# Optimization experiments

Measured on AMD Instinct MI355X. Metric: run time of the kernel, lower is better.

The kernel has to match this reference:

```python
import jax, jax.numpy as jnp
import numpy as np

B, S, D, H = 2, 2048, 2048, 16
HD = D // H
QMAX = 127.0  # 8-bit activation quant


def ste_round(x):
    # forward: round; backward: identity
    return x + jax.lax.stop_gradient(jnp.round(x) - x)


def bitlinear(x, w):
    """BitNet b1.58 linear: per-tensor ternary weights + per-token int8 activations.

    x: [..., in], w: [out, in] -> [..., out]
    """
    w_scale = jnp.maximum(jnp.mean(jnp.abs(w)), 1e-6)
    w_q = jnp.clip(ste_round(w / w_scale), -1.0, 1.0)          # ternary {-1,0,1}
    a_max = jnp.clip(jnp.max(jnp.abs(x), axis=-1, keepdims=True), 1e-8, None)
    x_q = jnp.clip(ste_round(x * (QMAX / a_max)), -QMAX, QMAX)  # int8 range
    y = jnp.einsum('bsi,oi->bso', x_q, w_q)
    return y * (w_scale * a_max / QMAX)


def setup_inputs() -> dict:
    key = jax.random.key(0)
    ks = jax.random.split(key, 5)
    std = 1.0 / np.sqrt(D)  # muP-style init from BitLinear
    return {
        'x': jax.random.normal(ks[0], (B, S, D), dtype=jnp.float32),
        'wq': jax.random.normal(ks[1], (D, D), dtype=jnp.float32) * std,
        'wk': jax.random.normal(ks[2], (D, D), dtype=jnp.float32) * std,
        'wv': jax.random.normal(ks[3], (D, D), dtype=jnp.float32) * std,
        'wo': jax.random.normal(ks[4], (D, D), dtype=jnp.float32) * std,
    }


def reference(x, wq, wk, wv, wo):
    q = bitlinear(x, wq).reshape(B, S, H, HD)
    k = bitlinear(x, wk).reshape(B, S, H, HD)
    v = bitlinear(x, wv).reshape(B, S, H, HD)
    scores = jnp.einsum('bqhd,bkhd->bhqk', q, k) / np.sqrt(HD)
    # causal mask
    causal = jnp.tril(jnp.ones((S, S), dtype=bool))
    scores = jnp.where(causal[None, None], scores, jnp.finfo(scores.dtype).min)
    attn = jax.nn.softmax(scores, axis=-1)
    ctx = jnp.einsum('bhqk,bkhd->bqhd', attn, v).reshape(B, S, D)
    return bitlinear(ctx, wo)
```

## Files before the change

kernel.cpp:

```cpp
#include <hip/hip_runtime.h>
#include <hip/hip_bf16.h>
#include <cstdint>
#include <cstddef>


#define BB 2
#define SS 2048
#define DD 2048
#define HH 16
#define HDD 128
#define MM (BB*SS)

typedef __attribute__((ext_vector_type(8))) short bf16x8;
typedef __attribute__((ext_vector_type(4))) float f32x4;
typedef __attribute__((ext_vector_type(16))) float f32x16;
typedef __attribute__((ext_vector_type(4))) int   i32x4;
typedef unsigned short u16;
typedef unsigned int   u32;
typedef unsigned char  u8;
typedef signed char    s8;

#define MFMA(a,b,c)   __builtin_amdgcn_mfma_f32_16x16x32_bf16(a,b,c,0,0,0)
#define MFMA32(a,b,c) __builtin_amdgcn_mfma_f32_32x32x16_bf16(a,b,c,0,0,0)
#define MFMAI8(a,b,c) __builtin_amdgcn_mfma_i32_16x16x64_i8(a,b,c,0,0,0)

static __device__ __forceinline__ u16 f2bf(float f) {
  u32 x = __float_as_uint(f);
  u32 r = x + 0x7fffu + ((x >> 16) & 1u);
  return (u16)(r >> 16);
}

static __device__ __forceinline__ void gl_lds16(const void* g, void* l) {
  __builtin_amdgcn_global_load_lds((const __attribute__((address_space(1))) void*)g,
                                   (__attribute__((address_space(3))) void*)l, 16, 0, 0);
}

__global__ void k_wabs_partial(const float* __restrict__ w0, const float* __restrict__ w1,
                               const float* __restrict__ w2, const float* __restrict__ w3,
                               double* __restrict__ part) {
  int m = blockIdx.x >> 8, blk = blockIdx.x & 255;
  const float* w = (m == 0) ? w0 : (m == 1) ? w1 : (m == 2) ? w2 : w3;
  const float* p = w + (size_t)blk * 16384;
  double s = 0.0;
  for (int i = threadIdx.x * 4; i < 16384; i += 1024) {
    float4 v = *(const float4*)(p + i);
    s += (double)fabsf(v.x) + (double)fabsf(v.y) + (double)fabsf(v.z) + (double)fabsf(v.w);
  }
  __shared__ double red[256];
  red[threadIdx.x] = s;
  __syncthreads();
  for (int off = 128; off > 0; off >>= 1) {
    if ((int)threadIdx.x < off) red[threadIdx.x] += red[threadIdx.x + off];
    __syncthreads();
  }
  if (threadIdx.x == 0) part[m * 256 + blk] = red[0];
}

__global__ void k_wscale_final(const double* __restrict__ part, float* __restrict__ scales) {
  int m = threadIdx.x;
  if (m < 4) {
    double s = 0.0;
    for (int i = 0; i < 256; i++) s += part[m * 256 + i];
    float v = (float)(s * (1.0 / 4194304.0));
    scales[m] = fmaxf(v, 1e-6f);
  }
}

__global__ void k_wquant(const float* __restrict__ w0, const float* __restrict__ w1,
                         const float* __restrict__ w2, const float* __restrict__ w3,
                         s8* __restrict__ wq, const float* __restrict__ scales) {
  int m = blockIdx.y;
  const float* w = (m == 0) ? w0 : (m == 1) ? w1 : (m == 2) ? w2 : w3;
  float ws = scales[m];
  size_t i = ((size_t)blockIdx.x * 256 + threadIdx.x) * 4;
  float4 v = *(const float4*)(w + i);
  s8 o[4];
  o[0] = (s8)(int)fminf(1.f, fmaxf(-1.f, rintf(v.x / ws)));
  o[1] = (s8)(int)fminf(1.f, fmaxf(-1.f, rintf(v.y / ws)));
  o[2] = (s8)(int)fminf(1.f, fmaxf(-1.f, rintf(v.z / ws)));
  o[3] = (s8)(int)fminf(1.f, fmaxf(-1.f, rintf(v.w / ws)));
  *(int*)(wq + (size_t)m * DD * DD + i) = *(const int*)o;
}

__global__ __launch_bounds__(256) void k_rowquant(const float* __restrict__ x, s8* __restrict__ xq,
                                                  float* __restrict__ amax) {
  int row = blockIdx.x, t = threadIdx.x;
  const float* p = x + (size_t)row * DD + t * 8;
  float4 v0 = *(const float4*)(p);
  float4 v1 = *(const float4*)(p + 4);
  float m = fmaxf(fmaxf(fmaxf(fabsf(v0.x), fabsf(v0.y)), fmaxf(fabsf(v0.z), fabsf(v0.w))),
                  fmaxf(fmaxf(fabsf(v1.x), fabsf(v1.y)), fmaxf(fabsf(v1.z), fabsf(v1.w))));
  m = fmaxf(m, __shfl_xor(m, 1));  m = fmaxf(m, __shfl_xor(m, 2));
  m = fmaxf(m, __shfl_xor(m, 4));  m = fmaxf(m, __shfl_xor(m, 8));
  m = fmaxf(m, __shfl_xor(m, 16)); m = fmaxf(m, __shfl_xor(m, 32));
  __shared__ float red[4];
  if ((t & 63) == 0) red[t >> 6] = m;
  __syncthreads();
  m = fmaxf(fmaxf(red[0], red[1]), fmaxf(red[2], red[3]));
  m = fmaxf(m, 1e-8f);
  if (t == 0) amax[row] = m;
  float s = 127.0f / m;
  s8 o[8];
  o[0] = (s8)(int)fminf(127.f, fmaxf(-127.f, rintf(v0.x * s)));
  o[1] = (s8)(int)fminf(127.f, fmaxf(-127.f, rintf(v0.y * s)));
  o[2] = (s8)(int)fminf(127.f, fmaxf(-127.f, rintf(v0.z * s)));
  o[3] = (s8)(int)fminf(127.f, fmaxf(-127.f, rintf(v0.w * s)));
  o[4] = (s8)(int)fminf(127.f, fmaxf(-127.f, rintf(v1.x * s)));
  o[5] = (s8)(int)fminf(127.f, fmaxf(-127.f, rintf(v1.y * s)));
  o[6] = (s8)(int)fminf(127.f, fmaxf(-127.f, rintf(v1.z * s)));
  o[7] = (s8)(int)fminf(127.f, fmaxf(-127.f, rintf(v1.w * s)));
  *(uint2*)(xq + (size_t)row * DD + t * 8) = *(const uint2*)o;
}

template<bool OB, int NBNL>
__global__ __launch_bounds__(512) void k_gemm(const s8* __restrict__ A, const s8* __restrict__ Bw,
                                              const float* __restrict__ amax,
                                              const float* __restrict__ scales, int sbase,
                                              void* __restrict__ outv) {
  __shared__ alignas(16) u8 Asm[2][128 * 128];
  __shared__ alignas(16) u8 Bsm[2][256 * 128];
  int id = blockIdx.x;
  int xcd = id & 7, kk = id >> 3;
  int bm = kk & 31, bn = xcd * NBNL + (kk >> 5);
  int t = threadIdx.x, w = t >> 6, l = t & 63;
  int wr = w >> 2, wc = w & 3;
  int l15 = l & 15, lh = l >> 4;
  int r0 = t >> 3;
  int c0 = ((t & 7) ^ (r0 & 7)) * 16;
  const s8* Ab = A  + (size_t)(bm * 128) * DD;
  const s8* Bb = Bw + (size_t)(bn * 256) * DD;

#define STG_A(tt) do { u8* d_ = &Asm[(tt) & 1][0];                                    \
    gl_lds16(Ab + (size_t)r0 * DD + (tt) * 128 + c0,        d_ + t * 16);             \
    gl_lds16(Ab + (size_t)(r0 + 64) * DD + (tt) * 128 + c0, d_ + (512 + t) * 16); } while (0)
#define STG_B(tt, h_) do { u8* d_ = &Bsm[(tt) & 1][(h_) * 16384];                     \
    gl_lds16(Bb + (size_t)((h_) * 128 + r0) * DD + (tt) * 128 + c0,        d_ + t * 16);\
    gl_lds16(Bb + (size_t)((h_) * 128 + r0 + 64) * DD + (tt) * 128 + c0,   d_ + (512 + t) * 16); } while (0)

  i32x4 acc[4][4] = {};
  STG_A(0); STG_B(0, 0); STG_B(0, 1); STG_B(1, 0);
  asm volatile("s_waitcnt vmcnt(2)" ::: "memory");
  asm volatile("s_barrier" ::: "memory");
  for (int kb = 0; kb < 16; kb++) {
    int b = kb & 1;
    const u8* Ac = &Asm[b][0];
    const u8* Bc = &Bsm[b][0];
    i32x4 af[4][2], bf[2][2];
    #pragma unroll
    for (int i = 0; i < 4; i++)
      #pragma unroll
      for (int ks = 0; ks < 2; ks++)
        af[i][ks] = *(const i32x4*)(Ac + (wr * 64 + i * 16 + l15) * 128 + (((ks * 4 + lh) ^ (l15 & 7)) * 16));
    #pragma unroll
    for (int j = 0; j < 2; j++)
      #pragma unroll
      for (int ks = 0; ks < 2; ks++)
        bf[j][ks] = *(const i32x4*)(Bc + ((wc + 4 * j) * 16 + l15) * 128 + (((ks * 4 + lh) ^ (l15 & 7)) * 16));
    if (kb + 1 < 16) { STG_A(kb + 1); STG_B(kb + 1, 1); }
    asm volatile("s_barrier" ::: "memory");
    asm volatile("s_waitcnt lgkmcnt(0)" ::: "memory");
    __builtin_amdgcn_sched_barrier(0);
    __builtin_amdgcn_s_setprio(1);
    #pragma unroll
    for (int ks = 0; ks < 2; ks++)
      #pragma unroll
      for (int i = 0; i < 4; i++)
        #pragma unroll
        for (int j = 0; j < 2; j++)
          acc[i][j] = MFMAI8(af[i][ks], bf[j][ks], acc[i][j]);
    __builtin_amdgcn_s_setprio(0);
    asm volatile("s_barrier" ::: "memory");
    i32x4 bg[2][2];
    #pragma unroll
    for (int j = 0; j < 2; j++)
      #pragma unroll
      for (int ks = 0; ks < 2; ks++)
        bg[j][ks] = *(const i32x4*)(Bc + ((wc + 4 * (2 + j)) * 16 + l15) * 128 + (((ks * 4 + lh) ^ (l15 & 7)) * 16));
    if (kb + 2 < 16) STG_B(kb + 2, 0);
    asm volatile("s_barrier" ::: "memory");
    asm volatile("s_waitcnt lgkmcnt(0)" ::: "memory");
    __builtin_amdgcn_sched_barrier(0);
    __builtin_amdgcn_s_setprio(1);
    #pragma unroll
    for (int ks = 0; ks < 2; ks++)
      #pragma unroll
      for (int i = 0; i < 4; i++)
        #pragma unroll
        for (int j = 0; j < 2; j++)
          acc[i][2 + j] = MFMAI8(af[i][ks], bg[j][ks], acc[i][2 + j]);
    __builtin_amdgcn_s_setprio(0);
    if (kb < 14) {
      asm volatile("s_waitcnt vmcnt(2)" ::: "memory");
      asm volatile("s_barrier" ::: "memory");
    } else if (kb == 14) {
      asm volatile("s_waitcnt vmcnt(0)" ::: "memory");
      asm volatile("s_barrier" ::: "memory");
    }
  }
#undef STG_A
#undef STG_B
  int mz = OB ? (bn >> 3) : 0;
  int lcol0 = OB ? ((bn & 7) * 256) : (bn * 256);
  float wsc = scales[sbase + mz];
  u16*   outb = (u16*)outv + (size_t)mz * MM * DD;
  float* outf = (float*)outv;
  #pragma unroll
  for (int i = 0; i < 4; i++) {
    int row0 = bm * 128 + wr * 64 + i * 16 + lh * 4;
    #pragma unroll
    for (int r = 0; r < 4; r++) {
      float sc = (wsc * amax[row0 + r]) / 127.0f;
      #pragma unroll
      for (int j = 0; j < 4; j++) {
        int col = lcol0 + (wc + 4 * j) * 16 + l15;
        float y = (float)acc[i][j][r] * sc;
        if (OB) outb[(size_t)(row0 + r) * DD + col] = f2bf(y);
        else    outf[(size_t)(row0 + r) * DD + col] = y;
      }
    }
  }
}

__global__ __launch_bounds__(256) void k_vtrans(const u16* __restrict__ v, u16* __restrict__ vt) {
  __shared__ u16 tile[64][72];
  int sb = blockIdx.x;
  int db = blockIdx.y;
  int bh = blockIdx.z;
  int b = bh >> 4, h = bh & 15;
  int t = threadIdx.x;
  int ls = t >> 2, ld0 = (t & 3) * 16;
  const u16* src = v + (size_t)(b * SS + sb * 64 + ls) * DD + h * HDD + db * 64 + ld0;
  *(int4*)(&tile[ls][ld0])     = *(const int4*)(src);
  *(int4*)(&tile[ls][ld0 + 8]) = *(const int4*)(src + 8);
  __syncthreads();
  int d = t >> 2, s0 = (t & 3) * 16;
  u16 tmp[16];
  #pragma unroll
  for (int k = 0; k < 16; k++) tmp[k] = tile[s0 + k][d];
  u16* dst = vt + (size_t)((bh * HDD) + db * 64 + d) * SS + sb * 64 + s0;
  *(int4*)(dst)     = *(const int4*)(tmp);
  *(int4*)(dst + 8) = *(const int4*)(tmp + 8);
}

__global__ __launch_bounds__(128) void k_attn(const u16* __restrict__ Q, const u16* __restrict__ K,
                                              const u16* __restrict__ VT, float* __restrict__ O) {
  __shared__ alignas(16) u16 Ks[2][64 * 128];
  __shared__ alignas(16) u16 Vs[2][128 * 64];
  __shared__ alignas(16) u16 Ps[2 * 32 * 64];
  int id = blockIdx.x;
  int bh = (id & 7) * 4 + ((id >> 3) & 3);
  int pr = id >> 5;
  int b = bh >> 4, h = bh & 15;
  int t = threadIdx.x, w = t >> 6, l = t & 63;
  int l31 = l & 31, hi = l >> 5;
  int l15 = l & 15, lh = l >> 4;
  size_t base = (size_t)(b * SS) * DD + h * HDD;
  const u16* vtb = VT + (size_t)bh * HDD * SS;
  u16* Ptw = Ps + w * 2048;
  const float sc2 = 0.12751944557270094f;
  int ksr[8], kso[8], vsr[8], vso[8];
  #pragma unroll
  for (int i = 0; i < 8; i++) {
    int s = i * 128 + t;
    ksr[i] = s >> 4; kso[i] = ((s & 15) ^ (ksr[i] & 15)) * 8;
    vsr[i] = s >> 3; vso[i] = ((s & 7) ^ (vsr[i] & 7)) * 8;
  }

#define ASTAGE(kb_, bf_) do {                                                           \
    _Pragma("unroll")                                                                   \
    for (int i_ = 0; i_ < 8; i_++)                                                      \
      gl_lds16(K + base + (size_t)((kb_) * 64 + ksr[i_]) * DD + kso[i_],                \
               &Ks[bf_][(i_ * 128 + t) * 8]);                                           \
    _Pragma("unroll")                                                                   \
    for (int i_ = 0; i_ < 8; i_++)                                                      \
      gl_lds16(vtb + (size_t)vsr[i_] * SS + (kb_) * 64 + vso[i_],                       \
               &Vs[bf_][(i_ * 128 + t) * 8]);                                           \
  } while (0)

  for (int half = 0; half < 2; half++) {
    int qt = half ? (31 - pr) : pr;
    int qrow = qt * 64 + w * 32 + l31;
    bf16x8 qf[8];
    #pragma unroll
    for (int kt = 0; kt < 8; kt++)
      qf[kt] = *(const bf16x8*)(Q + base + (size_t)qrow * DD + kt * 16 + hi * 8);
    f32x4 cacc[2][8] = {};
    float mrun = -INFINITY, lrun = 0.f;
    ASTAGE(0, 0);
    asm volatile("s_waitcnt vmcnt(0)" ::: "memory");
    asm volatile("s_barrier" ::: "memory");
    for (int kb = 0; kb <= qt; kb++) {
      int cur = kb & 1;
      if (kb < qt) ASTAGE(kb + 1, cur ^ 1);
      const u16* Kc = &Ks[cur][0];
      const u16* Vc = &Vs[cur][0];
      f32x16 c0 = {}, c1 = {};
      #pragma unroll
      for (int kt = 0; kt < 8; kt++) {
        int sl = (((kt * 2 + hi) ^ (l31 & 15)) * 8);
        bf16x8 kf0 = *(const bf16x8*)(Kc + l31 * 128 + sl);
        bf16x8 kf1 = *(const bf16x8*)(Kc + (32 + l31) * 128 + sl);
        c0 = MFMA32(kf0, qf[kt], c0);
        c1 = MFMA32(kf1, qf[kt], c1);
      }
      if (kb == qt) {
        #pragma unroll
        for (int rg = 0; rg < 16; rg++) {
          int kv0 = kb * 64 + (rg & 3) + 8 * (rg >> 2) + 4 * hi;
          if (kv0 > qrow)      c0[rg] = -1e30f;
          if (kv0 + 32 > qrow) c1[rg] = -1e30f;
        }
      }
      float ta[16];
      #pragma unroll
      for (int rg = 0; rg < 16; rg++) ta[rg] = fmaxf(c0[rg], c1[rg]);
      #pragma unroll
      for (int off = 8; off > 0; off >>= 1)
        #pragma unroll
        for (int rg = 0; rg < 8; rg++)
          if (rg < off) ta[rg] = fmaxf(ta[rg], ta[rg + off]);
      float pmax = fmaxf(ta[0], __shfl_xor(ta[0], 32));
      if (__any(pmax - mrun > 90.50967f)) {
        float mnew = fmaxf(mrun, pmax);
        float alpha = __builtin_amdgcn_exp2f((mrun - mnew) * sc2);
        lrun *= alpha;
        #pragma unroll
        for (int m16 = 0; m16 < 2; m16++)
          #pragma unroll
          for (int r = 0; r < 4; r++) {
            float ar = __shfl(alpha, m16 * 16 + lh * 4 + r);
            #pragma unroll
            for (int n2 = 0; n2 < 8; n2++) cacc[m16][n2][r] *= ar;
          }
        mrun = mnew;
      }
      float msc2 = mrun * sc2;
      float ts[16];
      #pragma unroll
      for (int rg = 0; rg < 16; rg++) {
        float p0 = __builtin_amdgcn_exp2f(fmaf(c0[rg], sc2, -msc2)); c0[rg] = p0;
        float p1 = __builtin_amdgcn_exp2f(fmaf(c1[rg], sc2, -msc2)); c1[rg] = p1;
        ts[rg] = p0 + p1;
      }
      #pragma unroll
      for (int off = 8; off > 0; off >>= 1)
        #pragma unroll
        for (int rg = 0; rg < 8; rg++)
          if (rg < off) ts[rg] += ts[rg + off];
      lrun += ts[0] + __shfl_xor(ts[0], 32);
      #pragma unroll
      for (int q4 = 0; q4 < 4; q4++) {
        uint2 pk0, pk1;
        pk0.x = (u32)f2bf(c0[4 * q4 + 0]) | ((u32)f2bf(c0[4 * q4 + 1]) << 16);
        pk0.y = (u32)f2bf(c0[4 * q4 + 2]) | ((u32)f2bf(c0[4 * q4 + 3]) << 16);
        pk1.x = (u32)f2bf(c1[4 * q4 + 0]) | ((u32)f2bf(c1[4 * q4 + 1]) << 16);
        pk1.y = (u32)f2bf(c1[4 * q4 + 2]) | ((u32)f2bf(c1[4 * q4 + 3]) << 16);
        *(uint2*)(Ptw + l31 * 64 + ((q4 ^ (l31 & 7)) * 8 + 4 * hi))       = pk0;
        *(uint2*)(Ptw + l31 * 64 + (((4 + q4) ^ (l31 & 7)) * 8 + 4 * hi)) = pk1;
      }
      #pragma unroll
      for (int ks = 0; ks < 2; ks++) {
        int so = ((ks * 4 + lh) ^ (l15 & 7)) * 8;
        bf16x8 pf0 = *(const bf16x8*)(Ptw + (l15) * 64 + so);
        bf16x8 pf1 = *(const bf16x8*)(Ptw + (16 + l15) * 64 + so);
        #pragma unroll
        for (int n2 = 0; n2 < 8; n2++) {
          bf16x8 vf = *(const bf16x8*)(Vc + (n2 * 16 + l15) * 64 + so);
          cacc[0][n2] = MFMA(pf0, vf, cacc[0][n2]);
          cacc[1][n2] = MFMA(pf1, vf, cacc[1][n2]);
        }
      }
      asm volatile("s_waitcnt vmcnt(0)" ::: "memory");
      asm volatile("s_barrier" ::: "memory");
    }
    float inv = 1.0f / lrun;
    #pragma unroll
    for (int m16 = 0; m16 < 2; m16++)
      #pragma unroll
      for (int r = 0; r < 4; r++) {
        float ir = __shfl(inv, m16 * 16 + lh * 4 + r);
        float* op = O + base + (size_t)(qt * 64 + w * 32 + m16 * 16 + lh * 4 + r) * DD;
        #pragma unroll
        for (int n2 = 0; n2 < 8; n2++)
          op[n2 * 16 + l15] = cacc[m16][n2][r] * ir;
      }
  }
#undef ASTAGE
}

extern "C" void kernel_launch(void* const* d_in, const int* in_sizes, int n_in,
                              void* d_out, int out_size, void* d_ws, size_t ws_size,
                              hipStream_t stream) {
  const float* x  = (const float*)d_in[0];
  const float* wq = (const float*)d_in[1];
  const float* wk = (const float*)d_in[2];
  const float* wv = (const float*)d_in[3];
  const float* wo = (const float*)d_in[4];
  char* ws = (char*)d_ws;
  float*  scales = (float*)(ws + 0);
  double* part   = (double*)(ws + 256);
  float*  amaxx  = (float*)(ws + 16384);
  float*  amaxc  = (float*)(ws + 49152);
  s8*     wqq    = (s8*)(ws + 131072);
  s8*     xq     = (s8*)(ws + 33685504);
  u16*    vt16   = (u16*)(ws + 33685504);
  u16*    qb     = (u16*)(ws + 50462720);
  u16*    kb     = (u16*)(ws + 67239936);
  u16*    vb     = (u16*)(ws + 84017152);
  float*  ctx    = (float*)(ws + 100794368);
  (void)in_sizes; (void)n_in; (void)out_size; (void)ws_size;

  k_wabs_partial<<<1024, 256, 0, stream>>>(wq, wk, wv, wo, part);
  k_wscale_final<<<1, 64, 0, stream>>>(part, scales);
  k_wquant<<<dim3(4096, 4), 256, 0, stream>>>(wq, wk, wv, wo, wqq, scales);
  k_rowquant<<<MM, 256, 0, stream>>>(x, xq, amaxx);
  k_gemm<true, 3><<<768, 512, 0, stream>>>(xq, wqq, amaxx, scales, 0, (void*)qb);
  k_vtrans<<<dim3(32, 2, 32), 256, 0, stream>>>(vb, vt16);
  k_attn<<<512, 128, 0, stream>>>(qb, kb, vt16, ctx);
  k_rowquant<<<MM, 256, 0, stream>>>(ctx, xq, amaxc);
  k_gemm<false, 1><<<256, 512, 0, stream>>>(xq, wqq + (size_t)3 * DD * DD, amaxc, scales, 3, d_out);
}
```

Before: 236.0 us.

## Store attention context as bf16, shrink output GEMM tile, use packed bf16 convert

```diff
diff --git a/kernel.cpp b/kernel.cpp
--- a/kernel.cpp
+++ b/kernel.cpp
@@ -28,6 +28,12 @@
   u32 x = __float_as_uint(f);
   u32 r = x + 0x7fffu + ((x >> 16) & 1u);
   return (u16)(r >> 16);
+}
+
+static __device__ __forceinline__ u32 cvtpk(float a, float b) {
+  u32 r;
+  asm("v_cvt_pk_bf16_f32 %0, %1, %2" : "=v"(r) : "v"(a), "v"(b));
+  return r;
 }
 
 static __device__ __forceinline__ void gl_lds16(const void* g, void* l) {
@@ -82,14 +88,27 @@
   *(int*)(wq + (size_t)m * DD * DD + i) = *(const int*)o;
 }
 
-__global__ __launch_bounds__(256) void k_rowquant(const float* __restrict__ x, s8* __restrict__ xq,
+template<bool BF16IN>
+__global__ __launch_bounds__(256) void k_rowquant(const void* __restrict__ xin, s8* __restrict__ xq,
                                                   float* __restrict__ amax) {
   int row = blockIdx.x, t = threadIdx.x;
-  const float* p = x + (size_t)row * DD + t * 8;
-  float4 v0 = *(const float4*)(p);
-  float4 v1 = *(const float4*)(p + 4);
-  float m = fmaxf(fmaxf(fmaxf(fabsf(v0.x), fabsf(v0.y)), fmaxf(fabsf(v0.z), fabsf(v0.w))),
-                  fmaxf(fmaxf(fabsf(v1.x), fabsf(v1.y)), fmaxf(fabsf(v1.z), fabsf(v1.w))));
+  float f[8];
+  if (BF16IN) {
+    const u16* p = (const u16*)xin + (size_t)row * DD + t * 8;
+    int4 v = *(const int4*)p;
+    const u16* pv = (const u16*)&v;
+    #pragma unroll
+    for (int i = 0; i < 8; i++) f[i] = __uint_as_float((u32)pv[i] << 16);
+  } else {
+    const float* p = (const float*)xin + (size_t)row * DD + t * 8;
+    float4 v0 = *(const float4*)(p);
+    float4 v1 = *(const float4*)(p + 4);
+    f[0] = v0.x; f[1] = v0.y; f[2] = v0.z; f[3] = v0.w;
+    f[4] = v1.x; f[5] = v1.y; f[6] = v1.z; f[7] = v1.w;
+  }
+  float m = 0.f;
+  #pragma unroll
+  for (int i = 0; i < 8; i++) m = fmaxf(m, fabsf(f[i]));
   m = fmaxf(m, __shfl_xor(m, 1));  m = fmaxf(m, __shfl_xor(m, 2));
   m = fmaxf(m, __shfl_xor(m, 4));  m = fmaxf(m, __shfl_xor(m, 8));
   m = fmaxf(m, __shfl_xor(m, 16)); m = fmaxf(m, __shfl_xor(m, 32));
@@ -101,24 +120,20 @@
   if (t == 0) amax[row] = m;
   float s = 127.0f / m;
   s8 o[8];
-  o[0] = (s8)(int)fminf(127.f, fmaxf(-127.f, rintf(v0.x * s)));
-  o[1] = (s8)(int)fminf(127.f, fmaxf(-127.f, rintf(v0.y * s)));
-  o[2] = (s8)(int)fminf(127.f, fmaxf(-127.f, rintf(v0.z * s)));
-  o[3] = (s8)(int)fminf(127.f, fmaxf(-127.f, rintf(v0.w * s)));
-  o[4] = (s8)(int)fminf(127.f, fmaxf(-127.f, rintf(v1.x * s)));
-  o[5] = (s8)(int)fminf(127.f, fmaxf(-127.f, rintf(v1.y * s)));
-  o[6] = (s8)(int)fminf(127.f, fmaxf(-127.f, rintf(v1.z * s)));
-  o[7] = (s8)(int)fminf(127.f, fmaxf(-127.f, rintf(v1.w * s)));
+  #pragma unroll
+  for (int i = 0; i < 8; i++)
+    o[i] = (s8)(int)fminf(127.f, fmaxf(-127.f, rintf(f[i] * s)));
   *(uint2*)(xq + (size_t)row * DD + t * 8) = *(const uint2*)o;
 }
 
-template<bool OB, int NBNL>
+template<bool OB, int NBNL, int BN>
 __global__ __launch_bounds__(512) void k_gemm(const s8* __restrict__ A, const s8* __restrict__ Bw,
                                               const float* __restrict__ amax,
                                               const float* __restrict__ scales, int sbase,
                                               void* __restrict__ outv) {
+  constexpr int NJ = BN / 128;
   __shared__ alignas(16) u8 Asm[2][128 * 128];
-  __shared__ alignas(16) u8 Bsm[2][256 * 128];
+  __shared__ alignas(16) u8 Bsm[2][BN * 128];
   int id = blockIdx.x;
   int xcd = id & 7, kk = id >> 3;
   int bm = kk & 31, bn = xcd * NBNL + (kk >> 5);
@@ -128,31 +143,38 @@
   int r0 = t >> 3;
   int c0 = ((t & 7) ^ (r0 & 7)) * 16;
   const s8* Ab = A  + (size_t)(bm * 128) * DD;
-  const s8* Bb = Bw + (size_t)(bn * 256) * DD;
-
-#define STG_A(tt) do { u8* d_ = &Asm[(tt) & 1][0];                                    \
-    gl_lds16(Ab + (size_t)r0 * DD + (tt) * 128 + c0,        d_ + t * 16);             \
-    gl_lds16(Ab + (size_t)(r0 + 64) * DD + (tt) * 128 + c0, d_ + (512 + t) * 16); } while (0)
-#define STG_B(tt, h_) do { u8* d_ = &Bsm[(tt) & 1][(h_) * 16384];                     \
-    gl_lds16(Bb + (size_t)((h_) * 128 + r0) * DD + (tt) * 128 + c0,        d_ + t * 16);\
-    gl_lds16(Bb + (size_t)((h_) * 128 + r0 + 64) * DD + (tt) * 128 + c0,   d_ + (512 + t) * 16); } while (0)
-
-  i32x4 acc[4][4] = {};
+  const s8* Bb = Bw + (size_t)(bn * BN) * DD;
+
+  auto STG_A = [&](int tt) {
+    u8* d_ = &Asm[tt & 1][0];
+    gl_lds16(Ab + (size_t)r0 * DD + tt * 128 + c0,        d_ + t * 16);
+    gl_lds16(Ab + (size_t)(r0 + 64) * DD + tt * 128 + c0, d_ + (512 + t) * 16);
+  };
+  auto STG_B = [&](int tt, int h_) {
+    u8* d_ = &Bsm[tt & 1][(size_t)h_ * (BN / 2) * 128];
+    #pragma unroll
+    for (int jj = 0; jj < NJ; jj++)
+      gl_lds16(Bb + (size_t)(h_ * (BN / 2) + jj * 64 + r0) * DD + tt * 128 + c0,
+               d_ + (jj * 512 + t) * 16);
+  };
+
+  i32x4 acc[4][2 * NJ] = {};
   STG_A(0); STG_B(0, 0); STG_B(0, 1); STG_B(1, 0);
-  asm volatile("s_waitcnt vmcnt(2)" ::: "memory");
+  if constexpr (NJ == 2) asm volatile("s_waitcnt vmcnt(2)" ::: "memory");
+  else                   asm volatile("s_waitcnt vmcnt(1)" ::: "memory");
   asm volatile("s_barrier" ::: "memory");
   for (int kb = 0; kb < 16; kb++) {
     int b = kb & 1;
     const u8* Ac = &Asm[b][0];
     const u8* Bc = &Bsm[b][0];
-    i32x4 af[4][2], bf[2][2];
+    i32x4 af[4][2], bf[NJ][2];
     #pragma unroll
     for (int i = 0; i < 4; i++)
       #pragma unroll
       for (int ks = 0; ks < 2; ks++)
         af[i][ks] = *(const i32x4*)(Ac + (wr * 64 + i * 16 + l15) * 128 + (((ks * 4 + lh) ^ (l15 & 7)) * 16));
     #pragma unroll
-    for (int j = 0; j < 2; j++)
+    for (int j = 0; j < NJ; j++)
       #pragma unroll
       for (int ks = 0; ks < 2; ks++)
         bf[j][ks] = *(const i32x4*)(Bc + ((wc + 4 * j) * 16 + l15) * 128 + (((ks * 4 + lh) ^ (l15 & 7)) * 16));
@@ -166,16 +188,16 @@
       #pragma unroll
       for (int i = 0; i < 4; i++)
         #pragma unroll
-        for (int j = 0; j < 2; j++)
+        for (int j = 0; j < NJ; j++)
           acc[i][j] = MFMAI8(af[i][ks], bf[j][ks], acc[i][j]);
     __builtin_amdgcn_s_setprio(0);
     asm volatile("s_barrier" ::: "memory");
-    i32x4 bg[2][2];
-    #pragma unroll
-    for (int j = 0; j < 2; j++)
+    i32x4 bg[NJ][2];
+    #pragma unroll
+    for (int j = 0; j < NJ; j++)
       #pragma unroll
       for (int ks = 0; ks < 2; ks++)
-        bg[j][ks] = *(const i32x4*)(Bc + ((wc + 4 * (2 + j)) * 16 + l15) * 128 + (((ks * 4 + lh) ^ (l15 & 7)) * 16));
+        bg[j][ks] = *(const i32x4*)(Bc + ((wc + 4 * (NJ + j)) * 16 + l15) * 128 + (((ks * 4 + lh) ^ (l15 & 7)) * 16));
     if (kb + 2 < 16) STG_B(kb + 2, 0);
     asm volatile("s_barrier" ::: "memory");
     asm volatile("s_waitcnt lgkmcnt(0)" ::: "memory");
@@ -186,21 +208,20 @@
       #pragma unroll
       for (int i = 0; i < 4; i++)
         #pragma unroll
-        for (int j = 0; j < 2; j++)
-          acc[i][2 + j] = MFMAI8(af[i][ks], bg[j][ks], acc[i][2 + j]);
+        for (int j = 0; j < NJ; j++)
+          acc[i][NJ + j] = MFMAI8(af[i][ks], bg[j][ks], acc[i][NJ + j]);
     __builtin_amdgcn_s_setprio(0);
     if (kb < 14) {
-      asm volatile("s_waitcnt vmcnt(2)" ::: "memory");
+      if constexpr (NJ == 2) asm volatile("s_waitcnt vmcnt(2)" ::: "memory");
+      else                   asm volatile("s_waitcnt vmcnt(1)" ::: "memory");
       asm volatile("s_barrier" ::: "memory");
     } else if (kb == 14) {
       asm volatile("s_waitcnt vmcnt(0)" ::: "memory");
       asm volatile("s_barrier" ::: "memory");
     }
   }
-#undef STG_A
-#undef STG_B
   int mz = OB ? (bn >> 3) : 0;
-  int lcol0 = OB ? ((bn & 7) * 256) : (bn * 256);
+  int lcol0 = OB ? ((bn & 7) * 256) : (bn * BN);
   float wsc = scales[sbase + mz];
   u16*   outb = (u16*)outv + (size_t)mz * MM * DD;
   float* outf = (float*)outv;
@@ -211,7 +232,7 @@
     for (int r = 0; r < 4; r++) {
       float sc = (wsc * amax[row0 + r]) / 127.0f;
       #pragma unroll
-      for (int j = 0; j < 4; j++) {
+      for (int j = 0; j < 2 * NJ; j++) {
         int col = lcol0 + (wc + 4 * j) * 16 + l15;
         float y = (float)acc[i][j][r] * sc;
         if (OB) outb[(size_t)(row0 + r) * DD + col] = f2bf(y);
@@ -243,7 +264,7 @@
 }
 
 __global__ __launch_bounds__(128) void k_attn(const u16* __restrict__ Q, const u16* __restrict__ K,
-                                              const u16* __restrict__ VT, float* __restrict__ O) {
+                                              const u16* __restrict__ VT, u16* __restrict__ O) {
   __shared__ alignas(16) u16 Ks[2][64 * 128];
   __shared__ alignas(16) u16 Vs[2][128 * 64];
   __shared__ alignas(16) u16 Ps[2 * 32 * 64];
@@ -351,10 +372,10 @@
       #pragma unroll
       for (int q4 = 0; q4 < 4; q4++) {
         uint2 pk0, pk1;
-        pk0.x = (u32)f2bf(c0[4 * q4 + 0]) | ((u32)f2bf(c0[4 * q4 + 1]) << 16);
-        pk0.y = (u32)f2bf(c0[4 * q4 + 2]) | ((u32)f2bf(c0[4 * q4 + 3]) << 16);
-        pk1.x = (u32)f2bf(c1[4 * q4 + 0]) | ((u32)f2bf(c1[4 * q4 + 1]) << 16);
-        pk1.y = (u32)f2bf(c1[4 * q4 + 2]) | ((u32)f2bf(c1[4 * q4 + 3]) << 16);
+        pk0.x = cvtpk(c0[4 * q4 + 0], c0[4 * q4 + 1]);
+        pk0.y = cvtpk(c0[4 * q4 + 2], c0[4 * q4 + 3]);
+        pk1.x = cvtpk(c1[4 * q4 + 0], c1[4 * q4 + 1]);
+        pk1.y = cvtpk(c1[4 * q4 + 2], c1[4 * q4 + 3]);
         *(uint2*)(Ptw + l31 * 64 + ((q4 ^ (l31 & 7)) * 8 + 4 * hi))       = pk0;
         *(uint2*)(Ptw + l31 * 64 + (((4 + q4) ^ (l31 & 7)) * 8 + 4 * hi)) = pk1;
       }
@@ -379,10 +400,10 @@
       #pragma unroll
       for (int r = 0; r < 4; r++) {
         float ir = __shfl(inv, m16 * 16 + lh * 4 + r);
-        float* op = O + base + (size_t)(qt * 64 + w * 32 + m16 * 16 + lh * 4 + r) * DD;
+        u16* op = O + base + (size_t)(qt * 64 + w * 32 + m16 * 16 + lh * 4 + r) * DD;
         #pragma unroll
         for (int n2 = 0; n2 < 8; n2++)
-          op[n2 * 16 + l15] = cacc[m16][n2][r] * ir;
+          op[n2 * 16 + l15] = f2bf(cacc[m16][n2][r] * ir);
       }
   }
 #undef ASTAGE
@@ -407,16 +428,16 @@
   u16*    qb     = (u16*)(ws + 50462720);
   u16*    kb     = (u16*)(ws + 67239936);
   u16*    vb     = (u16*)(ws + 84017152);
-  float*  ctx    = (float*)(ws + 100794368);
+  u16*    ctx    = (u16*)(ws + 100794368);
   (void)in_sizes; (void)n_in; (void)out_size; (void)ws_size;
 
   k_wabs_partial<<<1024, 256, 0, stream>>>(wq, wk, wv, wo, part);
   k_wscale_final<<<1, 64, 0, stream>>>(part, scales);
   k_wquant<<<dim3(4096, 4), 256, 0, stream>>>(wq, wk, wv, wo, wqq, scales);
-  k_rowquant<<<MM, 256, 0, stream>>>(x, xq, amaxx);
-  k_gemm<true, 3><<<768, 512, 0, stream>>>(xq, wqq, amaxx, scales, 0, (void*)qb);
+  k_rowquant<false><<<MM, 256, 0, stream>>>(x, xq, amaxx);
+  k_gemm<true, 3, 256><<<768, 512, 0, stream>>>(xq, wqq, amaxx, scales, 0, (void*)qb);
   k_vtrans<<<dim3(32, 2, 32), 256, 0, stream>>>(vb, vt16);
   k_attn<<<512, 128, 0, stream>>>(qb, kb, vt16, ctx);
-  k_rowquant<<<MM, 256, 0, stream>>>(ctx, xq, amaxc);
-  k_gemm<false, 1><<<256, 512, 0, stream>>>(xq, wqq + (size_t)3 * DD * DD, amaxc, scales, 3, d_out);
-}
+  k_rowquant<true><<<MM, 256, 0, stream>>>(ctx, xq, amaxc);
+  k_gemm<false, 2, 128><<<512, 512, 0, stream>>>(xq, wqq + (size_t)3 * DD * DD, amaxc, scales, 3, d_out);
+}
```

New measurement: 227.5 us. -3.6%, faster.
